# Kernel tuning notes

Measured on AMD Instinct MI355X. Metric: run time of the kernel, lower is better.

## Reference

```python
import jax, jax.numpy as jnp
import numpy as np

N, E = 100000, 1600000          # nodes, edges
DIN, DH, DOUT = 256, 128, 1      # input_dim, hidden_dim, output_dim


def _lin_init(k, din, dout):
    # mimic torch Linear init scale (values don't affect correctness testing)
    s = 1.0 / np.sqrt(din)
    kw, kb = jax.random.split(k)
    W = jax.random.uniform(kw, (din, dout), jnp.float32, -s, s)
    b = jax.random.uniform(kb, (dout,), jnp.float32, -s, s)
    return W, b


def setup_inputs() -> dict:
    key = jax.random.key(0)
    ks = jax.random.split(key, 6)
    x = jax.random.normal(ks[0], (N, DIN), dtype=jnp.float32)
    edge_index = jax.random.randint(ks[1], (2, E), 0, N, dtype=jnp.int64 if jax.config.jax_enable_x64 else jnp.int32)
    W1, b1 = _lin_init(ks[2], DIN, DH)
    W2, b2 = _lin_init(ks[3], DH, DH)
    W3, b3 = _lin_init(ks[4], DH, DH // 2)
    Wc, bc = _lin_init(ks[5], DH // 2, DOUT)
    return {"x": x, "edge_index": edge_index,
            "W1": W1, "b1": b1, "W2": W2, "b2": b2,
            "W3": W3, "b3": b3, "Wc": Wc, "bc": bc}


def _gcn_conv(x, W, b, src, dst, norm_e, norm_self):
    # PyG GCNConv: h = X W; out_i = sum_{j->i} norm_ij h_j + norm_ii h_i + b
    h = x @ W                                           # [N, dout]
    msgs = h[src] * norm_e[:, None]                     # [E, dout] gather
    agg = jax.ops.segment_sum(msgs, dst, num_segments=x.shape[0])  # scatter
    return agg + h * norm_self[:, None] + b


def reference(x, edge_index, W1, b1, W2, b2, W3, b3, Wc, bc):
    src, dst = edge_index[0], edge_index[1]
    n = x.shape[0]
    # symmetric GCN normalization with self-loops: deg = in-degree(A) + 1
    deg = jax.ops.segment_sum(jnp.ones(src.shape[0], x.dtype), dst, num_segments=n) + 1.0
    dinv = jax.lax.rsqrt(deg)
    norm_e = dinv[src] * dinv[dst]   # per-edge norm
    norm_self = dinv * dinv          # self-loop norm

    h = jax.nn.relu(_gcn_conv(x, W1, b1, src, dst, norm_e, norm_self))
    # dropout is identity in eval mode
    h = jax.nn.relu(_gcn_conv(h, W2, b2, src, dst, norm_e, norm_self))
    h = jax.nn.relu(_gcn_conv(h, W3, b3, src, dst, norm_e, norm_self))
    return h @ Wc + bc               # [N, 1]
```

## Files before the change

### kernel.cpp

```cpp
#include <hip/hip_runtime.h>
#include <cstdint>
#include <cstddef>

typedef __attribute__((ext_vector_type(4))) float f32x4;
typedef __attribute__((ext_vector_type(8))) _Float16 half8v;
typedef __attribute__((ext_vector_type(2))) _Float16 half2v;

static inline int cdiv(int a, int b){ return (a + b - 1) / b; }

#define BSH 9
#define CH 8192


__global__ __launch_bounds__(256) void wcvt_count_kernel(const float* __restrict__ W1, _Float16* __restrict__ W1t,
                                                         const float* __restrict__ W2, _Float16* __restrict__ W2t,
                                                         const float* __restrict__ W3, _Float16* __restrict__ W3t,
                                                         const int* __restrict__ dst, int* __restrict__ counts, int E){
  int b = blockIdx.x;
  if (b < 224){
    int i = b * 256 + threadIdx.x;
    if (b < 128){
      int k = i / 128, n = i & 127;
      W1t[(size_t)n * 256 + k] = (_Float16)W1[i];
    } else if (b < 192){
      int j = i - 128 * 256;
      int k = j / 128, n = j & 127;
      W2t[(size_t)n * 128 + k] = (_Float16)W2[j];
    } else {
      int j = i - 192 * 256;
      int k = j / 64, n = j & 63;
      W3t[(size_t)n * 128 + k] = (_Float16)W3[j];
    }
    return;
  }
  int cb = b - 224;
  int base = cb * 1024 + threadIdx.x;
  #pragma unroll
  for (int j = 0; j < 4; j++){
    int i = base + j * 256;
    if (i < E) atomicAdd(&counts[__builtin_nontemporal_load(dst + i)], 1);
  }
}


__global__ __launch_bounds__(256) void partial_dinv_kernel(const int* __restrict__ counts, int* __restrict__ bsum,
                                                           float* __restrict__ dinv, int n){
  __shared__ int sdata[256];
  int b = blockIdx.x, t = threadIdx.x;
  int base = b * 1024 + t * 4;
  int s = 0;
  #pragma unroll
  for (int i = 0; i < 4; i++){
    if (base + i < n){
      int c = counts[base + i];
      s += c;
      dinv[base + i] = rsqrtf((float)c + 1.0f);
    }
  }
  sdata[t] = s; __syncthreads();
  for (int off = 128; off > 0; off >>= 1){
    if (t < off) sdata[t] += sdata[t + off];
    __syncthreads();
  }
  if (t == 0) bsum[b] = sdata[0];
}

__global__ void scan_partials_kernel(const int* __restrict__ bsum, int* __restrict__ bsum_ex,
                                     int* __restrict__ row_off, int nblocks, int n){
  int run = 0;
  for (int i = 0; i < nblocks; i++){ bsum_ex[i] = run; run += bsum[i]; }
  row_off[n] = run;
}


__global__ __launch_bounds__(256) void scan_chunk_kernel(const int* __restrict__ counts, const int* __restrict__ bsum_ex,
                                                         int* __restrict__ row_off, int* __restrict__ bcur, int n){
  __shared__ int sdata[256];
  int b = blockIdx.x, t = threadIdx.x;
  int base = b * 1024 + t * 4;
  int c0 = (base + 0 < n) ? counts[base + 0] : 0;
  int c1 = (base + 1 < n) ? counts[base + 1] : 0;
  int c2 = (base + 2 < n) ? counts[base + 2] : 0;
  int c3 = (base + 3 < n) ? counts[base + 3] : 0;
  int tsum = c0 + c1 + c2 + c3;
  sdata[t] = tsum; __syncthreads();
  for (int off = 1; off < 256; off <<= 1){
    int v = (t >= off) ? sdata[t - off] : 0;
    __syncthreads();
    sdata[t] += v;
    __syncthreads();
  }
  int run = bsum_ex[b] + sdata[t] - tsum;
  if (base < n && (base & ((1 << BSH) - 1)) == 0) bcur[base >> BSH] = run;
  if (base + 0 < n){ row_off[base + 0] = run; run += c0; }
  if (base + 1 < n){ row_off[base + 1] = run; run += c1; }
  if (base + 2 < n){ row_off[base + 2] = run; run += c2; }
  if (base + 3 < n){ row_off[base + 3] = run; run += c3; }
}


__global__ __launch_bounds__(256) void bucket_scatter_kernel(const int* __restrict__ src, const int* __restrict__ dst,
                                                             int* __restrict__ bcur, unsigned* __restrict__ tmp,
                                                             int E, int NBK){
  __shared__ int hist[1024];
  __shared__ int hbase[1024];
  __shared__ unsigned pk[CH];
  __shared__ unsigned short bkt[CH];
  int t = threadIdx.x;
  int e0 = blockIdx.x * CH;
  int e1 = e0 + CH; if (e1 > E) e1 = E;
  int nloc = e1 - e0;
  for (int i = t; i < NBK; i += 256) hist[i] = 0;
  __syncthreads();
  for (int i = t; i < nloc; i += 256){
    int d = __builtin_nontemporal_load(dst + e0 + i);
    int s = __builtin_nontemporal_load(src + e0 + i);
    int b = d >> BSH;
    pk[i]  = ((unsigned)s << BSH) | (unsigned)(d & ((1 << BSH) - 1));
    bkt[i] = (unsigned short)b;
    atomicAdd(&hist[b], 1);
  }
  __syncthreads();
  for (int i = t; i < NBK; i += 256){
    int h = hist[i];
    hbase[i] = h ? atomicAdd(&bcur[i], h) : 0;
    hist[i] = 0;
  }
  __syncthreads();
  for (int i = t; i < nloc; i += 256){
    int b = bkt[i];
    int pos = atomicAdd(&hist[b], 1);
    tmp[hbase[b] + pos] = pk[i];
  }
}


__global__ __launch_bounds__(256) void bucket_sort_kernel(const unsigned* __restrict__ tmp, const int* __restrict__ row_off,
                                                          int* __restrict__ csr_src, int N){
  __shared__ int lcur[1 << BSH];
  int g = blockIdx.x;
  int base = g << BSH;
  int nloc = N - base; if (nloc > (1 << BSH)) nloc = (1 << BSH);
  int t = threadIdx.x;
  for (int i = t; i < nloc; i += 256) lcur[i] = row_off[base + i];
  __syncthreads();
  int rs = row_off[base], re = row_off[base + nloc];
  for (int i = rs + t; i < re; i += 256){
    unsigned v = tmp[i];
    int slot = atomicAdd(&lcur[v & ((1 << BSH) - 1)], 1);
    csr_src[slot] = (int)(v >> BSH);
  }
}


template<int BN, bool A32IN>
__global__ __launch_bounds__(256) void mgemm_kernel(const void* __restrict__ Ain, const _Float16* __restrict__ Bt,
                                                    _Float16* __restrict__ C16, const float* __restrict__ dscale,
                                                    int M, int K){
  constexpr int BM = 128, LD = 40;
  constexpr int MF = (BN == 128) ? 4 : 2;
  __shared__ _Float16 As[BM * LD];
  __shared__ _Float16 Bs[BN * LD];
  const float*    A32 = (const float*)Ain;
  const _Float16* A16 = (const _Float16*)Ain;
  int t = threadIdx.x;
  int w = t >> 6, l = t & 63;
  int m0 = blockIdx.x * BM;
  int wm = (BN == 128) ? (w >> 1) * 64 : w * 32;
  int wn = (BN == 128) ? (w & 1) * 64 : 0;
  int lr = l & 15;
  int kg = (l >> 4) * 8;

  f32x4 acc[MF][4];
  #pragma unroll
  for (int i = 0; i < MF; i++)
    #pragma unroll
    for (int j = 0; j < 4; j++){
      f32x4 z = {0.f, 0.f, 0.f, 0.f};
      acc[i][j] = z;
    }

  for (int k0 = 0; k0 < K; k0 += 32){
    __syncthreads();
    #pragma unroll
    for (int j = 0; j < (BM * 4) / 256; j++){
      int i = t + j * 256;
      int row = i >> 2, c = i & 3;
      int gr = m0 + row;
      half8v hv = {(_Float16)0, (_Float16)0, (_Float16)0, (_Float16)0,
                   (_Float16)0, (_Float16)0, (_Float16)0, (_Float16)0};
      if (gr < M){
        if (A32IN){
          const float* ap = A32 + (size_t)gr * K + k0 + c * 8;
          float4 f0 = *reinterpret_cast<const float4*>(ap);
          float4 f1 = *reinterpret_cast<const float4*>(ap + 4);
          hv[0] = (_Float16)f0.x; hv[1] = (_Float16)f0.y; hv[2] = (_Float16)f0.z; hv[3] = (_Float16)f0.w;
          hv[4] = (_Float16)f1.x; hv[5] = (_Float16)f1.y; hv[6] = (_Float16)f1.z; hv[7] = (_Float16)f1.w;
        } else {
          hv = *reinterpret_cast<const half8v*>(A16 + (size_t)gr * K + k0 + c * 8);
        }
      }
      *reinterpret_cast<half8v*>(&As[row * LD + c * 8]) = hv;
    }
    #pragma unroll
    for (int j = 0; j < (BN * 4) / 256; j++){
      int i = t + j * 256;
      int row = i >> 2, c = i & 3;
      *reinterpret_cast<half8v*>(&Bs[row * LD + c * 8]) =
        *reinterpret_cast<const half8v*>(Bt + (size_t)row * K + k0 + c * 8);
    }
    __syncthreads();
    half8v af[MF];
    #pragma unroll
    for (int mf = 0; mf < MF; mf++)
      af[mf] = *reinterpret_cast<const half8v*>(&As[(wm + mf * 16 + lr) * LD + kg]);
    #pragma unroll
    for (int nf = 0; nf < 4; nf++){
      half8v bf = *reinterpret_cast<const half8v*>(&Bs[(wn + nf * 16 + lr) * LD + kg]);
      #pragma unroll
      for (int mf = 0; mf < MF; mf++)
        acc[mf][nf] = __builtin_amdgcn_mfma_f32_16x16x32_f16(af[mf], bf, acc[mf][nf], 0, 0, 0);
    }
  }
  #pragma unroll
  for (int mf = 0; mf < MF; mf++){
    #pragma unroll
    for (int r = 0; r < 4; r++){
      int row = m0 + wm + mf * 16 + (l >> 4) * 4 + r;
      if (row < M){
        float sc = dscale[row];
        #pragma unroll
        for (int nf = 0; nf < 4; nf++)
          C16[(size_t)row * BN + wn + nf * 16 + lr] = (_Float16)(sc * acc[mf][nf][r]);
      }
    }
  }
}


__global__ __launch_bounds__(256) void agg128h_kernel(const _Float16* __restrict__ h16, const int* __restrict__ row_off,
                                                      const int* __restrict__ csr_src, const float* __restrict__ dinv,
                                                      const float* __restrict__ bias, _Float16* __restrict__ out16, int n){
  int node = blockIdx.x * 4 + (threadIdx.x >> 6);
  if (node >= n) return;
  int lane = threadIdx.x & 63;
  int e = row_off[node], eend = row_off[node + 1];
  float di = dinv[node];
  half2v sv = *reinterpret_cast<const half2v*>(h16 + (size_t)node * 128 + lane * 2);
  float ax = (float)sv[0], ay = (float)sv[1];
  while (e < eend){
    int m = eend - e; if (m > 64) m = 64;
    int idx = (lane < m) ? csr_src[e + lane] : 0;
    int i = 0;
    for (; i + 16 <= m; i += 16){
      half2v v[16];
      #pragma unroll
      for (int j = 0; j < 16; j++){
        int s = __shfl(idx, i + j);
        v[j] = *reinterpret_cast<const half2v*>(h16 + (size_t)s * 128 + lane * 2);
      }
      #pragma unroll
      for (int j = 0; j < 16; j++){ ax += (float)v[j][0]; ay += (float)v[j][1]; }
    }
    for (; i + 4 <= m; i += 4){
      half2v v[4];
      #pragma unroll
      for (int j = 0; j < 4; j++){
        int s = __shfl(idx, i + j);
        v[j] = *reinterpret_cast<const half2v*>(h16 + (size_t)s * 128 + lane * 2);
      }
      #pragma unroll
      for (int j = 0; j < 4; j++){ ax += (float)v[j][0]; ay += (float)v[j][1]; }
    }
    for (; i < m; i++){
      int s = __shfl(idx, i);
      half2v v = *reinterpret_cast<const half2v*>(h16 + (size_t)s * 128 + lane * 2);
      ax += (float)v[0]; ay += (float)v[1];
    }
    e += m;
  }
  float2 bv = *reinterpret_cast<const float2*>(bias + lane * 2);
  float ox = fmaxf(fmaf(di, ax, bv.x), 0.f);
  float oy = fmaxf(fmaf(di, ay, bv.y), 0.f);
  half2v o; o[0] = (_Float16)ox; o[1] = (_Float16)oy;
  *reinterpret_cast<half2v*>(out16 + (size_t)node * 128 + lane * 2) = o;
}


__global__ __launch_bounds__(256) void agg64h_cls_kernel(const _Float16* __restrict__ h16, const int* __restrict__ row_off,
                                                         const int* __restrict__ csr_src, const float* __restrict__ dinv,
                                                         const float* __restrict__ bias, const float* __restrict__ Wc,
                                                         const float* __restrict__ bc, float* __restrict__ out, int n){
  int node = blockIdx.x * 4 + (threadIdx.x >> 6);
  if (node >= n) return;
  int lane = threadIdx.x & 63;
  int e = row_off[node], eend = row_off[node + 1];
  float di = dinv[node];
  float a = (float)h16[(size_t)node * 64 + lane];
  while (e < eend){
    int m = eend - e; if (m > 64) m = 64;
    int idx = (lane < m) ? csr_src[e + lane] : 0;
    int i = 0;
    for (; i + 16 <= m; i += 16){
      _Float16 v[16];
      #pragma unroll
      for (int j = 0; j < 16; j++){
        int s = __shfl(idx, i + j);
        v[j] = h16[(size_t)s * 64 + lane];
      }
      #pragma unroll
      for (int j = 0; j < 16; j++) a += (float)v[j];
    }
    for (; i + 4 <= m; i += 4){
      _Float16 v[4];
      #pragma unroll
      for (int j = 0; j < 4; j++){
        int s = __shfl(idx, i + j);
        v[j] = h16[(size_t)s * 64 + lane];
      }
      #pragma unroll
      for (int j = 0; j < 4; j++) a += (float)v[j];
    }
    for (; i < m; i++){
      int s = __shfl(idx, i);
      a += (float)h16[(size_t)s * 64 + lane];
    }
    e += m;
  }
  float o = fmaxf(fmaf(di, a, bias[lane]), 0.f);
  float v = o * Wc[lane];
  #pragma unroll
  for (int off = 32; off > 0; off >>= 1) v += __shfl_down(v, off);
  if (lane == 0) out[node] = v + bc[0];
}


extern "C" void kernel_launch(void* const* d_in, const int* in_sizes, int n_in,
                              void* d_out, int out_size, void* d_ws, size_t ws_size,
                              hipStream_t stream){
  const float* x  = (const float*)d_in[0];
  const int*   ei = (const int*)d_in[1];
  const float* W1 = (const float*)d_in[2];
  const float* b1 = (const float*)d_in[3];
  const float* W2 = (const float*)d_in[4];
  const float* b2 = (const float*)d_in[5];
  const float* W3 = (const float*)d_in[6];
  const float* b3 = (const float*)d_in[7];
  const float* Wc = (const float*)d_in[8];
  const float* bc = (const float*)d_in[9];
  float* out = (float*)d_out;

  int N = in_sizes[0] / 256;
  int E = in_sizes[1] / 2;
  const int* src = ei;
  const int* dst = ei + E;
  int NBK = (N + (1 << BSH) - 1) >> BSH;

  char* ws = (char*)d_ws;
  size_t off = 0;
  auto alloc = [&](size_t bytes) -> char* {
    char* p = ws + off;
    off += (bytes + 511) & ~(size_t)511;
    return p;
  };
  int*      counts  = (int*)     alloc((size_t)N * 4);
  float*    dinv    = (float*)   alloc((size_t)N * 4);
  int*      row_off = (int*)     alloc(((size_t)N + 1) * 4);
  int*      bsum    = (int*)     alloc(1024);
  int*      bsum_ex = (int*)     alloc(1024);
  int*      bcur    = (int*)     alloc((size_t)NBK * 4);
  unsigned* tmp     = (unsigned*)alloc((size_t)E * 4);
  int*      csr_src = (int*)     alloc((size_t)E * 4);
  _Float16* bufH    = (_Float16*)alloc((size_t)N * 128 * 2);
  _Float16* bufG    = (_Float16*)alloc((size_t)N * 128 * 2);
  _Float16* W1t     = (_Float16*)alloc((size_t)256 * 128 * 2);
  _Float16* W2t     = (_Float16*)alloc((size_t)128 * 128 * 2);
  _Float16* W3t     = (_Float16*)alloc((size_t)128 * 64 * 2);

  int NB = (N + 1023) / 1024;

  hipMemsetAsync(counts, 0, (size_t)N * 4, stream);
  wcvt_count_kernel<<<224 + cdiv(E, 1024), 256, 0, stream>>>(W1, W1t, W2, W2t, W3, W3t, dst, counts, E);
  partial_dinv_kernel<<<NB, 256, 0, stream>>>(counts, bsum, dinv, N);
  scan_partials_kernel<<<1, 1, 0, stream>>>(bsum, bsum_ex, row_off, NB, N);
  scan_chunk_kernel<<<NB, 256, 0, stream>>>(counts, bsum_ex, row_off, bcur, N);
  bucket_scatter_kernel<<<cdiv(E, CH), 256, 0, stream>>>(src, dst, bcur, tmp, E, NBK);
  bucket_sort_kernel<<<NBK, 256, 0, stream>>>(tmp, row_off, csr_src, N);
  mgemm_kernel<128, true ><<<cdiv(N, 128), 256, 0, stream>>>(x, W1t, bufH, dinv, N, 256);
  agg128h_kernel<<<cdiv(N, 4), 256, 0, stream>>>(bufH, row_off, csr_src, dinv, b1, bufG, N);
  mgemm_kernel<128, false><<<cdiv(N, 128), 256, 0, stream>>>(bufG, W2t, bufH, dinv, N, 128);
  agg128h_kernel<<<cdiv(N, 4), 256, 0, stream>>>(bufH, row_off, csr_src, dinv, b2, bufG, N);
  mgemm_kernel<64, false><<<cdiv(N, 128), 256, 0, stream>>>(bufG, W3t, bufH, dinv, N, 128);
  agg64h_cls_kernel<<<cdiv(N, 4), 256, 0, stream>>>(bufH, row_off, csr_src, dinv, b3, Wc, bc, out, N);
}
```

Measured before the change: 369.7 us.

## Replace per-node degree count and global scan with bucket-level histogram and in-bucket CSR build

The per-node global atomic degree count, the multi-pass node-level prefix scan and the single-thread partial scan are replaced. Only bucket-level counts are now computed, using shared-memory histograms. Per-node degrees, dinv and row offsets are derived inside each bucket's sort block from a local histogram and scan. This cuts global atomics on 100k counters, several kernel launches and a serial scan. In exchange, the sort kernel reads tmp twice and assumes NBK is at most 256 for the single-block scan.

```diff
diff --git a/kernel.cpp b/kernel.cpp
--- a/kernel.cpp
+++ b/kernel.cpp
@@ -10,15 +10,18 @@
 
 #define BSH 9
 #define CH 8192
-
-
-__global__ __launch_bounds__(256) void wcvt_count_kernel(const float* __restrict__ W1, _Float16* __restrict__ W1t,
+#define HCH 8192
+
+
+__global__ __launch_bounds__(256) void wcvt_bhist_kernel(const float* __restrict__ W1, _Float16* __restrict__ W1t,
                                                          const float* __restrict__ W2, _Float16* __restrict__ W2t,
                                                          const float* __restrict__ W3, _Float16* __restrict__ W3t,
-                                                         const int* __restrict__ dst, int* __restrict__ counts, int E){
-  int b = blockIdx.x;
+                                                         const int* __restrict__ dst, int* __restrict__ bktcnt,
+                                                         int E, int NBK){
+  __shared__ int hist[1024];
+  int b = blockIdx.x, t = threadIdx.x;
   if (b < 224){
-    int i = b * 256 + threadIdx.x;
+    int i = b * 256 + t;
     if (b < 128){
       int k = i / 128, n = i & 127;
       W1t[(size_t)n * 256 + k] = (_Float16)W1[i];
@@ -34,68 +37,41 @@
     return;
   }
   int cb = b - 224;
-  int base = cb * 1024 + threadIdx.x;
-  #pragma unroll
-  for (int j = 0; j < 4; j++){
-    int i = base + j * 256;
-    if (i < E) atomicAdd(&counts[__builtin_nontemporal_load(dst + i)], 1);
-  }
-}
-
-
-__global__ __launch_bounds__(256) void partial_dinv_kernel(const int* __restrict__ counts, int* __restrict__ bsum,
-                                                           float* __restrict__ dinv, int n){
+  for (int i = t; i < NBK; i += 256) hist[i] = 0;
+  __syncthreads();
+  int e0 = cb * HCH;
+  int e1 = e0 + HCH; if (e1 > E) e1 = E;
+  for (int i = e0 + t; i < e1; i += 256){
+    int d = __builtin_nontemporal_load(dst + i);
+    atomicAdd(&hist[d >> BSH], 1);
+  }
+  __syncthreads();
+  for (int i = t; i < NBK; i += 256){
+    int h = hist[i];
+    if (h) atomicAdd(&bktcnt[i], h);
+  }
+}
+
+
+__global__ __launch_bounds__(256) void bucket_scan_kernel(const int* __restrict__ bktcnt, int* __restrict__ bbase,
+                                                          int* __restrict__ bcur, int NBK, int E){
   __shared__ int sdata[256];
-  int b = blockIdx.x, t = threadIdx.x;
-  int base = b * 1024 + t * 4;
-  int s = 0;
-  #pragma unroll
-  for (int i = 0; i < 4; i++){
-    if (base + i < n){
-      int c = counts[base + i];
-      s += c;
-      dinv[base + i] = rsqrtf((float)c + 1.0f);
-    }
-  }
-  sdata[t] = s; __syncthreads();
-  for (int off = 128; off > 0; off >>= 1){
-    if (t < off) sdata[t] += sdata[t + off];
-    __syncthreads();
-  }
-  if (t == 0) bsum[b] = sdata[0];
-}
-
-__global__ void scan_partials_kernel(const int* __restrict__ bsum, int* __restrict__ bsum_ex,
-                                     int* __restrict__ row_off, int nblocks, int n){
-  int run = 0;
-  for (int i = 0; i < nblocks; i++){ bsum_ex[i] = run; run += bsum[i]; }
-  row_off[n] = run;
-}
-
-
-__global__ __launch_bounds__(256) void scan_chunk_kernel(const int* __restrict__ counts, const int* __restrict__ bsum_ex,
-                                                         int* __restrict__ row_off, int* __restrict__ bcur, int n){
-  __shared__ int sdata[256];
-  int b = blockIdx.x, t = threadIdx.x;
-  int base = b * 1024 + t * 4;
-  int c0 = (base + 0 < n) ? counts[base + 0] : 0;
-  int c1 = (base + 1 < n) ? counts[base + 1] : 0;
-  int c2 = (base + 2 < n) ? counts[base + 2] : 0;
-  int c3 = (base + 3 < n) ? counts[base + 3] : 0;
-  int tsum = c0 + c1 + c2 + c3;
-  sdata[t] = tsum; __syncthreads();
+  int t = threadIdx.x;
+  int c = (t < NBK) ? bktcnt[t] : 0;
+  sdata[t] = c;
+  __syncthreads();
   for (int off = 1; off < 256; off <<= 1){
     int v = (t >= off) ? sdata[t - off] : 0;
     __syncthreads();
     sdata[t] += v;
     __syncthreads();
   }
-  int run = bsum_ex[b] + sdata[t] - tsum;
-  if (base < n && (base & ((1 << BSH) - 1)) == 0) bcur[base >> BSH] = run;
-  if (base + 0 < n){ row_off[base + 0] = run; run += c0; }
-  if (base + 1 < n){ row_off[base + 1] = run; run += c1; }
-  if (base + 2 < n){ row_off[base + 2] = run; run += c2; }
-  if (base + 3 < n){ row_off[base + 3] = run; run += c3; }
+  if (t < NBK){
+    int ex = sdata[t] - c;
+    bbase[t] = ex;
+    bcur[t] = ex;
+  }
+  if (t == 0) bbase[NBK] = E;
 }
 
 
@@ -135,19 +111,47 @@
 }
 
 
-__global__ __launch_bounds__(256) void bucket_sort_kernel(const unsigned* __restrict__ tmp, const int* __restrict__ row_off,
-                                                          int* __restrict__ csr_src, int N){
-  __shared__ int lcur[1 << BSH];
+__global__ __launch_bounds__(256) void bucket_build_kernel(const unsigned* __restrict__ tmp, const int* __restrict__ bbase,
+                                                           int* __restrict__ row_off, float* __restrict__ dinv,
+                                                           int* __restrict__ csr_src, int N, int E, int NBK){
+  __shared__ int hist[512];
+  __shared__ int sdata[256];
+  __shared__ int lofs[512];
   int g = blockIdx.x;
   int base = g << BSH;
-  int nloc = N - base; if (nloc > (1 << BSH)) nloc = (1 << BSH);
+  int nloc = N - base; if (nloc > 512) nloc = 512;
   int t = threadIdx.x;
-  for (int i = t; i < nloc; i += 256) lcur[i] = row_off[base + i];
-  __syncthreads();
-  int rs = row_off[base], re = row_off[base + nloc];
+  int rs = bbase[g], re = bbase[g + 1];
+  hist[t] = 0; hist[t + 256] = 0;
+  __syncthreads();
+  for (int i = rs + t; i < re; i += 256)
+    atomicAdd(&hist[tmp[i] & 511], 1);
+  __syncthreads();
+  int h0 = hist[2 * t], h1 = hist[2 * t + 1];
+  int pairsum = h0 + h1;
+  sdata[t] = pairsum;
+  __syncthreads();
+  for (int off = 1; off < 256; off <<= 1){
+    int v = (t >= off) ? sdata[t - off] : 0;
+    __syncthreads();
+    sdata[t] += v;
+    __syncthreads();
+  }
+  int ex = sdata[t] - pairsum;
+  lofs[2 * t] = ex;
+  lofs[2 * t + 1] = ex + h0;
+  __syncthreads();
+  for (int j = t; j < nloc; j += 256){
+    dinv[base + j] = rsqrtf((float)hist[j] + 1.0f);
+    row_off[base + j] = rs + lofs[j];
+  }
+  if (g == NBK - 1 && t == 0) row_off[N] = E;
+  __syncthreads();
+  for (int j = t; j < 512; j += 256) hist[j] = rs + lofs[j];
+  __syncthreads();
   for (int i = rs + t; i < re; i += 256){
     unsigned v = tmp[i];
-    int slot = atomicAdd(&lcur[v & ((1 << BSH) - 1)], 1);
+    int slot = atomicAdd(&hist[v & 511], 1);
     csr_src[slot] = (int)(v >> BSH);
   }
 }
@@ -363,12 +367,11 @@
     off += (bytes + 511) & ~(size_t)511;
     return p;
   };
-  int*      counts  = (int*)     alloc((size_t)N * 4);
+  int*      bktcnt  = (int*)     alloc((size_t)NBK * 4);
+  int*      bbase   = (int*)     alloc(((size_t)NBK + 1) * 4);
+  int*      bcur    = (int*)     alloc((size_t)NBK * 4);
   float*    dinv    = (float*)   alloc((size_t)N * 4);
   int*      row_off = (int*)     alloc(((size_t)N + 1) * 4);
-  int*      bsum    = (int*)     alloc(1024);
-  int*      bsum_ex = (int*)     alloc(1024);
-  int*      bcur    = (int*)     alloc((size_t)NBK * 4);
   unsigned* tmp     = (unsigned*)alloc((size_t)E * 4);
   int*      csr_src = (int*)     alloc((size_t)E * 4);
   _Float16* bufH    = (_Float16*)alloc((size_t)N * 128 * 2);
@@ -377,15 +380,11 @@
   _Float16* W2t     = (_Float16*)alloc((size_t)128 * 128 * 2);
   _Float16* W3t     = (_Float16*)alloc((size_t)128 * 64 * 2);
 
-  int NB = (N + 1023) / 1024;
-
-  hipMemsetAsync(counts, 0, (size_t)N * 4, stream);
-  wcvt_count_kernel<<<224 + cdiv(E, 1024), 256, 0, stream>>>(W1, W1t, W2, W2t, W3, W3t, dst, counts, E);
-  partial_dinv_kernel<<<NB, 256, 0, stream>>>(counts, bsum, dinv, N);
-  scan_partials_kernel<<<1, 1, 0, stream>>>(bsum, bsum_ex, row_off, NB, N);
-  scan_chunk_kernel<<<NB, 256, 0, stream>>>(counts, bsum_ex, row_off, bcur, N);
+  hipMemsetAsync(bktcnt, 0, (size_t)NBK * 4, stream);
+  wcvt_bhist_kernel<<<224 + cdiv(E, HCH), 256, 0, stream>>>(W1, W1t, W2, W2t, W3, W3t, dst, bktcnt, E, NBK);
+  bucket_scan_kernel<<<1, 256, 0, stream>>>(bktcnt, bbase, bcur, NBK, E);
   bucket_scatter_kernel<<<cdiv(E, CH), 256, 0, stream>>>(src, dst, bcur, tmp, E, NBK);
-  bucket_sort_kernel<<<NBK, 256, 0, stream>>>(tmp, row_off, csr_src, N);
+  bucket_build_kernel<<<NBK, 256, 0, stream>>>(tmp, bbase, row_off, dinv, csr_src, N, E, NBK);
   mgemm_kernel<128, true ><<<cdiv(N, 128), 256, 0, stream>>>(x, W1t, bufH, dinv, N, 256);
   agg128h_kernel<<<cdiv(N, 4), 256, 0, stream>>>(bufH, row_off, csr_src, dinv, b1, bufG, N);
   mgemm_kernel<128, false><<<cdiv(N, 128), 256, 0, stream>>>(bufG, W2t, bufH, dinv, N, 128);
```

Result: faster. 317.6 us (-14.1%).
